# Kernel tuning notes

Measured on AMD Instinct MI355X. Metric: run time of the kernel, lower is better.

The kernel has to match this reference:

```python
import jax, jax.numpy as jnp
import numpy as np

GAMMA = 0.002  # Gaussian kernel bandwidth (init_kwargs)


def setup_inputs() -> dict:
    key = jax.random.key(0)
    k1, k2 = jax.random.split(key)
    x = jax.random.normal(k1, (4096, 512), dtype=jnp.float32)   # queries [B, D]
    sv = jax.random.normal(k2, (8192, 512), dtype=jnp.float32)  # centers [N, D]
    return {"x": x, "sv": sv}


def reference(x, sv):
    # Gaussian (RBF) kernel matrix: K[b, n] = exp(-gamma * ||x_b - sv_n||^2)
    # original chunked broadcast-subtract-square loop (same math, fused).
    x2 = jnp.sum(x * x, axis=-1)            # [B]
    s2 = jnp.sum(sv * sv, axis=-1)          # [N]
    cross = jnp.einsum('bd,nd->bn', x, sv)  # [B, N]
    d2 = x2[:, None] + s2[None, :] - 2.0 * cross
    return jnp.exp(-GAMMA * d2)
```

## Files before the change

kernel.cpp:

```cpp
#include <hip/hip_runtime.h>
#include <hip/hip_bf16.h>
#include <stdint.h>

#define GAMMA 0.002f
#define MDIM 4096
#define NDIM 8192
#define KDIM 512
#define BM 128
#define BN 128
#define BK 32

typedef short v8s __attribute__((ext_vector_type(8)));
typedef float v4f __attribute__((ext_vector_type(4)));

__device__ __forceinline__ unsigned short f32_to_bf16_rne(float f) {
    union { float f; uint32_t u; } v; v.f = f;
    uint32_t u = v.u;
    return (unsigned short)((u + 0x7fffu + ((u >> 16) & 1u)) >> 16);
}

__device__ __forceinline__ void gl_lds16(const void* g, void* l) {
    __builtin_amdgcn_global_load_lds(
        (const __attribute__((address_space(1))) uint32_t*)g,
        (__attribute__((address_space(3))) uint32_t*)l, 16, 0, 0);
}

__global__ __launch_bounds__(256) void convert_rows(
    const float* __restrict__ in, unsigned short* __restrict__ outb,
    float* __restrict__ neg_g_sq) {
    int row = blockIdx.x;
    const float* src = in + (size_t)row * KDIM;
    unsigned short* dst = outb + (size_t)row * KDIM;
    int t = threadIdx.x;
    float2 f = ((const float2*)src)[t];
    ushort2 b;
    b.x = f32_to_bf16_rne(f.x);
    b.y = f32_to_bf16_rne(f.y);
    ((ushort2*)dst)[t] = b;
    float s = f.x * f.x + f.y * f.y;
    #pragma unroll
    for (int off = 32; off > 0; off >>= 1) s += __shfl_down(s, off, 64);
    __shared__ float red[4];
    if ((t & 63) == 0) red[t >> 6] = s;
    __syncthreads();
    if (t == 0) neg_g_sq[row] = -GAMMA * (red[0] + red[1] + red[2] + red[3]);
}

__global__ __launch_bounds__(256) void rbf_gemm(
    const unsigned short* __restrict__ A,
    const unsigned short* __restrict__ B,
    const float* __restrict__ arow,
    const float* __restrict__ ccol,
    float* __restrict__ out) {

    __shared__ __align__(16) unsigned short sA[BM * BK];
    __shared__ __align__(16) unsigned short sB[BN * BK];

    const int tid  = threadIdx.x;
    const int lane = tid & 63;
    const int wave = tid >> 6;
    const int wm   = wave >> 1;
    const int wn   = wave & 1;
    const int row0 = blockIdx.y * BM;
    const int col0 = blockIdx.x * BN;

    const unsigned short* aptr = A + (size_t)(row0 + (tid >> 2)) * KDIM + (tid & 3) * 8;
    const unsigned short* bptr = B + (size_t)(col0 + (tid >> 2)) * KDIM + (tid & 3) * 8;
    unsigned short* sAp = &sA[tid * 8];
    unsigned short* sBp = &sB[tid * 8];

    v4f acc[4][4];
    #pragma unroll
    for (int i = 0; i < 4; i++)
        #pragma unroll
        for (int j = 0; j < 4; j++) acc[i][j] = (v4f)0.0f;

    const int q    = lane >> 4;
    const int r16  = lane & 15;

    for (int k0 = 0; k0 < KDIM; k0 += BK) {
        gl_lds16(aptr + k0, sAp);
        gl_lds16(aptr + (size_t)64 * KDIM + k0, sAp + 2048);
        gl_lds16(bptr + k0, sBp);
        gl_lds16(bptr + (size_t)64 * KDIM + k0, sBp + 2048);
        __syncthreads();

        v8s afrag[4], bfrag[4];
        #pragma unroll
        for (int i = 0; i < 4; i++) {
            afrag[i] = *(const v8s*)&sA[(wm * 64 + i * 16 + r16) * BK + q * 8];
            bfrag[i] = *(const v8s*)&sB[(wn * 64 + i * 16 + r16) * BK + q * 8];
        }
        #pragma unroll
        for (int i = 0; i < 4; i++)
            #pragma unroll
            for (int j = 0; j < 4; j++)
                acc[i][j] = __builtin_amdgcn_mfma_f32_16x16x32_bf16(
                    afrag[i], bfrag[j], acc[i][j], 0, 0, 0);
        __syncthreads();
    }

    float* fA = (float*)sA;
    float* fC = (float*)sB;
    if (tid < 128) fA[tid] = arow[row0 + tid];
    else           fC[tid - 128] = ccol[col0 + tid - 128];
    __syncthreads();

    const float tg = 2.0f * GAMMA;
    #pragma unroll
    for (int i = 0; i < 4; i++) {
        #pragma unroll
        for (int j = 0; j < 4; j++) {
            const int rbase = wm * 64 + i * 16 + q * 4;
            const int cl    = wn * 64 + j * 16 + r16;
            const float cc  = fC[cl];
            float* gp = out + (size_t)(row0 + rbase) * NDIM + (col0 + cl);
            #pragma unroll
            for (int v = 0; v < 4; v++) {
                gp[(size_t)v * NDIM] = __expf(fmaf(tg, acc[i][j][v], fA[rbase + v] + cc));
            }
        }
    }
}

extern "C" void kernel_launch(void* const* d_in, const int* in_sizes, int n_in,
                              void* d_out, int out_size, void* d_ws, size_t ws_size,
                              hipStream_t stream) {
    const float* x  = (const float*)d_in[0];
    const float* sv = (const float*)d_in[1];
    float* out = (float*)d_out;

    unsigned short* xb  = (unsigned short*)d_ws;
    unsigned short* svb = xb + (size_t)MDIM * KDIM;
    float* arow = (float*)(svb + (size_t)NDIM * KDIM);
    float* ccol = arow + MDIM;

    hipLaunchKernelGGL(convert_rows, dim3(MDIM), dim3(256), 0, stream, x, xb, arow);
    hipLaunchKernelGGL(convert_rows, dim3(NDIM), dim3(256), 0, stream, sv, svb, ccol);
    hipLaunchKernelGGL(rbf_gemm, dim3(NDIM / BN, MDIM / BM), dim3(256), 0, stream,
                       xb, svb, arow, ccol, out);
}
```

Baseline: 188.7 us.

## Rewrite RBF GEMM as 256x256 tile double-buffered pipelined kernel with swizzled LDS

Replaces the 128x128 single-buffer GEMM with a 256x256 tile, 512-thread kernel. It uses BK=64 double buffering via global_load_lds with interleaved stage issues, an XOR-swizzled LDS layout to avoid bank conflicts, and s_setprio around MFMA clusters. Blocks are remapped along a 1D grid for L2 locality, and the epilogue is transposed so each lane writes vectorized 16-byte stores. This aims to overlap loads with compute and cut the per-K-step barrier stalls. The costs are heavy register use for 32 accumulators, a 128KB LDS footprint, and manual vmcnt bookkeeping that must match exactly.

```diff
diff --git a/kernel.cpp b/kernel.cpp
--- a/kernel.cpp
+++ b/kernel.cpp
@@ -1,14 +1,10 @@
 #include <hip/hip_runtime.h>
-#include <hip/hip_bf16.h>
 #include <stdint.h>
 
 #define GAMMA 0.002f
 #define MDIM 4096
 #define NDIM 8192
 #define KDIM 512
-#define BM 128
-#define BN 128
-#define BK 32
 
 typedef short v8s __attribute__((ext_vector_type(8)));
 typedef float v4f __attribute__((ext_vector_type(4)));
@@ -46,79 +42,148 @@
     if (t == 0) neg_g_sq[row] = -GAMMA * (red[0] + red[1] + red[2] + red[3]);
 }
 
-__global__ __launch_bounds__(256) void rbf_gemm(
+#define QUAD(MH, NH)                                                          \
+  do {                                                                        \
+    __builtin_amdgcn_s_setprio(1);                                            \
+    _Pragma("unroll")                                                         \
+    for (int kk = 0; kk < 2; ++kk) {                                          \
+      _Pragma("unroll")                                                       \
+      for (int i2 = 0; i2 < 4; ++i2) {                                        \
+        _Pragma("unroll")                                                     \
+        for (int j2 = 0; j2 < 2; ++j2) {                                      \
+          acc[(MH)*4 + i2][(NH)*2 + j2] =                                     \
+              __builtin_amdgcn_mfma_f32_16x16x32_bf16(                        \
+                  bf[(NH)*2 + j2][kk], af[i2][kk],                            \
+                  acc[(MH)*4 + i2][(NH)*2 + j2], 0, 0, 0);                    \
+        }                                                                     \
+      }                                                                       \
+    }                                                                         \
+    __builtin_amdgcn_s_setprio(0);                                            \
+  } while (0)
+
+__global__ __launch_bounds__(512, 2) void rbf_gemm(
     const unsigned short* __restrict__ A,
     const unsigned short* __restrict__ B,
     const float* __restrict__ arow,
     const float* __restrict__ ccol,
     float* __restrict__ out) {
 
-    __shared__ __align__(16) unsigned short sA[BM * BK];
-    __shared__ __align__(16) unsigned short sB[BN * BK];
+    __shared__ __align__(16) char smem[131072];
 
     const int tid  = threadIdx.x;
     const int lane = tid & 63;
     const int wave = tid >> 6;
-    const int wm   = wave >> 1;
-    const int wn   = wave & 1;
-    const int row0 = blockIdx.y * BM;
-    const int col0 = blockIdx.x * BN;
-
-    const unsigned short* aptr = A + (size_t)(row0 + (tid >> 2)) * KDIM + (tid & 3) * 8;
-    const unsigned short* bptr = B + (size_t)(col0 + (tid >> 2)) * KDIM + (tid & 3) * 8;
-    unsigned short* sAp = &sA[tid * 8];
-    unsigned short* sBp = &sB[tid * 8];
-
-    v4f acc[4][4];
-    #pragma unroll
-    for (int i = 0; i < 4; i++)
-        #pragma unroll
-        for (int j = 0; j < 4; j++) acc[i][j] = (v4f)0.0f;
-
-    const int q    = lane >> 4;
-    const int r16  = lane & 15;
-
-    for (int k0 = 0; k0 < KDIM; k0 += BK) {
-        gl_lds16(aptr + k0, sAp);
-        gl_lds16(aptr + (size_t)64 * KDIM + k0, sAp + 2048);
-        gl_lds16(bptr + k0, sBp);
-        gl_lds16(bptr + (size_t)64 * KDIM + k0, sBp + 2048);
-        __syncthreads();
-
-        v8s afrag[4], bfrag[4];
-        #pragma unroll
-        for (int i = 0; i < 4; i++) {
-            afrag[i] = *(const v8s*)&sA[(wm * 64 + i * 16 + r16) * BK + q * 8];
-            bfrag[i] = *(const v8s*)&sB[(wn * 64 + i * 16 + r16) * BK + q * 8];
-        }
-        #pragma unroll
-        for (int i = 0; i < 4; i++)
+    const int wm   = wave >> 2;
+    const int wn   = wave & 3;
+
+    const int bid  = blockIdx.x;
+    const int swz  = ((bid & 7) << 6) | (bid >> 3);
+    const int row0 = (swz >> 5) << 8;
+    const int col0 = (swz & 31) << 8;
+
+    const int rA   = tid >> 3;
+    const int colS = ((tid & 7) << 4) ^ ((rA & 7) << 4);
+    const char* aSrc = (const char*)A + ((size_t)(row0 + rA) << 10) + colS;
+    const char* bSrc = (const char*)B + ((size_t)(col0 + rA) << 10) + colS;
+
+    auto stageA = [&](int tt, int h) {
+        const char* s = aSrc + tt * 128 + h * 131072;
+        char* d = smem + ((tt & 1) << 16) + h * 16384 + tid * 16;
+        gl_lds16(s, d);
+        gl_lds16(s + 65536, d + 8192);
+    };
+    auto stageB = [&](int tt, int h) {
+        const char* s = bSrc + tt * 128 + h * 131072;
+        char* d = smem + ((tt & 1) << 16) + 32768 + h * 16384 + tid * 16;
+        gl_lds16(s, d);
+        gl_lds16(s + 65536, d + 8192);
+    };
+
+    const int l15   = lane & 15;
+    const int colK0 = ((lane >> 4) ^ (lane & 7)) << 4;
+    const int aBase0 = wm * 16384 + l15 * 128 + colK0;
+    const int aBase1 = aBase0 ^ 64;
+    const int bBase0 = 32768 + (wn >> 1) * 16384 + (wn & 1) * 8192
+                       + l15 * 128 + colK0;
+    const int bBase1 = bBase0 ^ 64;
+
+    v4f acc[8][4];
+    #pragma unroll
+    for (int i = 0; i < 8; ++i)
+        #pragma unroll
+        for (int j = 0; j < 4; ++j) acc[i][j] = (v4f)0.0f;
+
+    v8s af[4][2];
+    v8s bf[4][2];
+
+    stageB(0, 0); stageB(0, 1); stageA(0, 0); stageA(0, 1);
+    stageB(1, 0); stageB(1, 1); stageA(1, 0);
+    asm volatile("s_waitcnt vmcnt(6)" ::: "memory");
+    __builtin_amdgcn_s_barrier();
+
+    #pragma unroll
+    for (int t = 0; t < 8; ++t) {
+        const int bufo = (t & 1) << 16;
+        #pragma unroll
+        for (int i2 = 0; i2 < 4; ++i2) {
+            af[i2][0] = *(const v8s*)(smem + bufo + aBase0 + i2 * 2048);
+            af[i2][1] = *(const v8s*)(smem + bufo + aBase1 + i2 * 2048);
+        }
+        #pragma unroll
+        for (int j = 0; j < 4; ++j) {
+            bf[j][0] = *(const v8s*)(smem + bufo + bBase0 + j * 2048);
+            bf[j][1] = *(const v8s*)(smem + bufo + bBase1 + j * 2048);
+        }
+        if (t + 1 < 8) stageA(t + 1, 1);
+        __builtin_amdgcn_s_barrier();
+        __builtin_amdgcn_sched_barrier(0);
+        QUAD(0, 0);
+        __builtin_amdgcn_s_barrier();
+        if (t + 2 < 8) stageB(t + 2, 0);
+        __builtin_amdgcn_s_barrier();
+        __builtin_amdgcn_sched_barrier(0);
+        QUAD(0, 1);
+        __builtin_amdgcn_s_barrier();
+        #pragma unroll
+        for (int i2 = 0; i2 < 4; ++i2) {
+            af[i2][0] = *(const v8s*)(smem + bufo + aBase0 + 8192 + i2 * 2048);
+            af[i2][1] = *(const v8s*)(smem + bufo + aBase1 + 8192 + i2 * 2048);
+        }
+        if (t + 2 < 8) stageB(t + 2, 1);
+        __builtin_amdgcn_s_barrier();
+        __builtin_amdgcn_sched_barrier(0);
+        QUAD(1, 0);
+        __builtin_amdgcn_s_barrier();
+        if (t + 2 < 8) stageA(t + 2, 0);
+        __builtin_amdgcn_s_barrier();
+        __builtin_amdgcn_sched_barrier(0);
+        QUAD(1, 1);
+        if (t < 6)       asm volatile("s_waitcnt vmcnt(6)" ::: "memory");
+        else if (t == 6) asm volatile("s_waitcnt vmcnt(0)" ::: "memory");
+        __builtin_amdgcn_s_barrier();
+    }
+
+    float* sb = (float*)smem;
+    if (tid < 256) sb[tid] = arow[row0 + tid];
+    else           sb[tid] = ccol[col0 + tid - 256];
+    __syncthreads();
+
+    const float tg = 2.0f * GAMMA;
+    const int g4 = (lane >> 4) << 2;
+    #pragma unroll
+    for (int i = 0; i < 8; ++i) {
+        const int r_l = wm * 128 + i * 16 + l15;
+        const float ra = sb[r_l];
+        float* gp = out + (size_t)(row0 + r_l) * NDIM + (col0 + wn * 64 + g4);
+        #pragma unroll
+        for (int j = 0; j < 4; ++j) {
+            v4f o;
             #pragma unroll
-            for (int j = 0; j < 4; j++)
-                acc[i][j] = __builtin_amdgcn_mfma_f32_16x16x32_bf16(
-                    afrag[i], bfrag[j], acc[i][j], 0, 0, 0);
-        __syncthreads();
-    }
-
-    float* fA = (float*)sA;
-    float* fC = (float*)sB;
-    if (tid < 128) fA[tid] = arow[row0 + tid];
-    else           fC[tid - 128] = ccol[col0 + tid - 128];
-    __syncthreads();
-
-    const float tg = 2.0f * GAMMA;
-    #pragma unroll
-    for (int i = 0; i < 4; i++) {
-        #pragma unroll
-        for (int j = 0; j < 4; j++) {
-            const int rbase = wm * 64 + i * 16 + q * 4;
-            const int cl    = wn * 64 + j * 16 + r16;
-            const float cc  = fC[cl];
-            float* gp = out + (size_t)(row0 + rbase) * NDIM + (col0 + cl);
-            #pragma unroll
-            for (int v = 0; v < 4; v++) {
-                gp[(size_t)v * NDIM] = __expf(fmaf(tg, acc[i][j][v], fA[rbase + v] + cc));
+            for (int v = 0; v < 4; ++v) {
+                const int c_l = wn * 64 + j * 16 + g4 + v;
+                o[v] = __expf(fmaf(tg, acc[i][j][v], ra + sb[256 + c_l]));
             }
+            *(v4f*)(gp + j * 16) = o;
         }
     }
 }
@@ -137,6 +202,6 @@
 
     hipLaunchKernelGGL(convert_rows, dim3(MDIM), dim3(256), 0, stream, x, xb, arow);
     hipLaunchKernelGGL(convert_rows, dim3(NDIM), dim3(256), 0, stream, sv, svb, ccol);
-    hipLaunchKernelGGL(rbf_gemm, dim3(NDIM / BN, MDIM / BM), dim3(256), 0, stream,
-                       xb, svb, arow, ccol, out);
-}
+    hipLaunchKernelGGL(rbf_gemm, dim3((MDIM / 256) * (NDIM / 256)), dim3(512), 0,
+                       stream, xb, svb, arow, ccol, out);
+}
```

New measurement: 187.7 us. Within noise of the previous version (-0.5%).

## Triple-buffer GEMM loads, swizzle LDS, remap blocks, and stage output through LDS

Applied to the files above, without the earlier changes.

Replaces the single-buffered K loop with a three-stage LDS ring that prefetches two tiles ahead, using explicit vmcnt waits and a single barrier per step. The LDS layout gets an XOR swizzle to avoid bank conflicts, and blocks are remapped through a 1D swizzled grid for L2 reuse. The epilogue computes exp in registers, then transposes through LDS so rows are written with coalesced 16-byte stores. This raises LDS use to about 49KB per block and relies on hand-tuned waitcnt ordering, which makes correctness more fragile.

```diff
diff --git a/kernel.cpp b/kernel.cpp
--- a/kernel.cpp
+++ b/kernel.cpp
@@ -1,14 +1,10 @@
 #include <hip/hip_runtime.h>
-#include <hip/hip_bf16.h>
 #include <stdint.h>
 
 #define GAMMA 0.002f
 #define MDIM 4096
 #define NDIM 8192
 #define KDIM 512
-#define BM 128
-#define BN 128
-#define BK 32
 
 typedef short v8s __attribute__((ext_vector_type(8)));
 typedef float v4f __attribute__((ext_vector_type(4)));
@@ -46,80 +42,125 @@
     if (t == 0) neg_g_sq[row] = -GAMMA * (red[0] + red[1] + red[2] + red[3]);
 }
 
-__global__ __launch_bounds__(256) void rbf_gemm(
+__global__ __launch_bounds__(256, 3) void rbf_gemm(
     const unsigned short* __restrict__ A,
     const unsigned short* __restrict__ B,
     const float* __restrict__ arow,
     const float* __restrict__ ccol,
     float* __restrict__ out) {
 
-    __shared__ __align__(16) unsigned short sA[BM * BK];
-    __shared__ __align__(16) unsigned short sB[BN * BK];
+    __shared__ __align__(16) char smem[50176];
 
     const int tid  = threadIdx.x;
     const int lane = tid & 63;
     const int wave = tid >> 6;
     const int wm   = wave >> 1;
     const int wn   = wave & 1;
-    const int row0 = blockIdx.y * BM;
-    const int col0 = blockIdx.x * BN;
 
-    const unsigned short* aptr = A + (size_t)(row0 + (tid >> 2)) * KDIM + (tid & 3) * 8;
-    const unsigned short* bptr = B + (size_t)(col0 + (tid >> 2)) * KDIM + (tid & 3) * 8;
-    unsigned short* sAp = &sA[tid * 8];
-    unsigned short* sBp = &sB[tid * 8];
+    const int bid  = blockIdx.x;
+    const int swz  = ((bid & 7) << 8) | (bid >> 3);
+    const int row0 = (swz & 31) << 7;
+    const int col0 = (swz >> 5) << 7;
+
+    const int rS  = tid >> 2;
+    const int cSw = ((tid & 3) << 4) ^ ((rS & 3) << 4);
+    const char* aS = (const char*)A + ((size_t)(row0 + rS) << 10) + cSw;
+    const char* bS = (const char*)B + ((size_t)(col0 + rS) << 10) + cSw;
+    char* dA = smem + tid * 16;
+    char* dB = smem + 8192 + tid * 16;
+
+    #define STAGE(t)                                                          \
+      do {                                                                    \
+        const int _b = ((t) % 3) * 16384;                                     \
+        const char* _sa = aS + (t) * 64;                                      \
+        const char* _sb = bS + (t) * 64;                                      \
+        gl_lds16(_sa,          dA + _b);                                      \
+        gl_lds16(_sa + 65536,  dA + _b + 4096);                               \
+        gl_lds16(_sb,          dB + _b);                                      \
+        gl_lds16(_sb + 65536,  dB + _b + 4096);                               \
+      } while (0)
+
+    const int q   = lane >> 4;
+    const int l15 = lane & 15;
+    const int ra0 = wm * 64 + l15;
+    const int aOff = ra0 * 64 + (((q << 4)) ^ ((ra0 & 3) << 4));
+    const int rb0 = wn * 64 + l15;
+    const int bOff = 8192 + rb0 * 64 + (((q << 4)) ^ ((rb0 & 3) << 4));
 
     v4f acc[4][4];
     #pragma unroll
-    for (int i = 0; i < 4; i++)
+    for (int i = 0; i < 4; ++i)
         #pragma unroll
-        for (int j = 0; j < 4; j++) acc[i][j] = (v4f)0.0f;
+        for (int j = 0; j < 4; ++j) acc[i][j] = (v4f)0.0f;
 
-    const int q    = lane >> 4;
-    const int r16  = lane & 15;
+    STAGE(0); STAGE(1);
+    if (tid < 128) ((float*)(smem + 49152))[tid] = arow[row0 + tid];
+    else           ((float*)(smem + 49664))[tid - 128] = ccol[col0 + tid - 128];
+    asm volatile("s_waitcnt vmcnt(4)" ::: "memory");
+    __builtin_amdgcn_s_barrier();
 
-    for (int k0 = 0; k0 < KDIM; k0 += BK) {
-        gl_lds16(aptr + k0, sAp);
-        gl_lds16(aptr + (size_t)64 * KDIM + k0, sAp + 2048);
-        gl_lds16(bptr + k0, sBp);
-        gl_lds16(bptr + (size_t)64 * KDIM + k0, sBp + 2048);
-        __syncthreads();
+    #pragma unroll
+    for (int t = 0; t < 16; ++t) {
+        if (t + 2 < 16) STAGE(t + 2);
+        const int bo = (t % 3) * 16384;
+        v8s af[4], bf[4];
+        #pragma unroll
+        for (int i = 0; i < 4; ++i) af[i] = *(const v8s*)(smem + bo + aOff + i * 1024);
+        #pragma unroll
+        for (int j = 0; j < 4; ++j) bf[j] = *(const v8s*)(smem + bo + bOff + j * 1024);
+        __builtin_amdgcn_s_setprio(1);
+        #pragma unroll
+        for (int i = 0; i < 4; ++i)
+            #pragma unroll
+            for (int j = 0; j < 4; ++j)
+                acc[i][j] = __builtin_amdgcn_mfma_f32_16x16x32_bf16(
+                    bf[j], af[i], acc[i][j], 0, 0, 0);
+        __builtin_amdgcn_s_setprio(0);
+        if (t < 14)      asm volatile("s_waitcnt vmcnt(4)" ::: "memory");
+        else if (t == 14) asm volatile("s_waitcnt vmcnt(0)" ::: "memory");
+        __builtin_amdgcn_s_barrier();
+    }
+    #undef STAGE
 
-        v8s afrag[4], bfrag[4];
+    const float tg = 2.0f * GAMMA;
+    const float* sbr = (const float*)(smem + 49152);
+    const float* sbc = (const float*)(smem + 49664);
+    #pragma unroll
+    for (int i = 0; i < 4; ++i) {
+        const float ra = sbr[wm * 64 + i * 16 + l15];
         #pragma unroll
-        for (int i = 0; i < 4; i++) {
-            afrag[i] = *(const v8s*)&sA[(wm * 64 + i * 16 + r16) * BK + q * 8];
-            bfrag[i] = *(const v8s*)&sB[(wn * 64 + i * 16 + r16) * BK + q * 8];
+        for (int j = 0; j < 4; ++j) {
+            #pragma unroll
+            for (int v = 0; v < 4; ++v) {
+                const int c_l = wn * 64 + j * 16 + (q << 2) + v;
+                acc[i][j][v] = __expf(fmaf(tg, acc[i][j][v], ra + sbc[c_l]));
+            }
         }
-        #pragma unroll
-        for (int i = 0; i < 4; i++)
-            #pragma unroll
-            for (int j = 0; j < 4; j++)
-                acc[i][j] = __builtin_amdgcn_mfma_f32_16x16x32_bf16(
-                    afrag[i], bfrag[j], acc[i][j], 0, 0, 0);
-        __syncthreads();
     }
 
-    float* fA = (float*)sA;
-    float* fC = (float*)sB;
-    if (tid < 128) fA[tid] = arow[row0 + tid];
-    else           fC[tid - 128] = ccol[col0 + tid - 128];
-    __syncthreads();
-
-    const float tg = 2.0f * GAMMA;
+    float* tb = (float*)smem;
     #pragma unroll
-    for (int i = 0; i < 4; i++) {
-        #pragma unroll
-        for (int j = 0; j < 4; j++) {
-            const int rbase = wm * 64 + i * 16 + q * 4;
-            const int cl    = wn * 64 + j * 16 + r16;
-            const float cc  = fC[cl];
-            float* gp = out + (size_t)(row0 + rbase) * NDIM + (col0 + cl);
+    for (int ch = 0; ch < 2; ++ch) {
+        if (wm == ch) {
             #pragma unroll
-            for (int v = 0; v < 4; v++) {
-                gp[(size_t)v * NDIM] = __expf(fmaf(tg, acc[i][j][v], fA[rbase + v] + cc));
+            for (int i = 0; i < 4; ++i) {
+                const int rl = i * 16 + l15;
+                #pragma unroll
+                for (int j = 0; j < 4; ++j) {
+                    const int g = wn * 16 + j * 4 + q;
+                    *(v4f*)&tb[rl * 128 + ((g ^ (rl & 31)) << 2)] = acc[i][j];
+                }
             }
         }
+        __syncthreads();
+        #pragma unroll
+        for (int rr = 0; rr < 8; ++rr) {
+            const int rl = wave * 16 + (rr << 1) + (lane >> 5);
+            v4f val = *(const v4f*)&tb[rl * 128 + (((lane & 31) ^ (rl & 31)) << 2)];
+            *(v4f*)(out + (size_t)(row0 + ch * 64 + rl) * NDIM + col0 +
+                    ((lane & 31) << 2)) = val;
+        }
+        __syncthreads();
     }
 }
 
@@ -137,6 +178,6 @@
 
     hipLaunchKernelGGL(convert_rows, dim3(MDIM), dim3(256), 0, stream, x, xb, arow);
     hipLaunchKernelGGL(convert_rows, dim3(NDIM), dim3(256), 0, stream, sv, svb, ccol);
-    hipLaunchKernelGGL(rbf_gemm, dim3(NDIM / BN, MDIM / BM), dim3(256), 0, stream,
-                       xb, svb, arow, ccol, out);
+    hipLaunchKernelGGL(rbf_gemm, dim3((MDIM / 128) * (NDIM / 128)), dim3(256), 0,
+                       stream, xb, svb, arow, ccol, out);
 }
```

Measured after the change: 187.0 us. About the same (-0.9%).
